# Performance work log

Measured on AMD Instinct MI355X. Metric: run time of the kernel, lower is better.

Reference implementation:

```python
import jax, jax.numpy as jnp
import numpy as np

NEG = 0.01  # torch leaky_relu default slope


def conv1d(x, w, pad):
    # x: [B, C, L], w: [O, I, K], stride 1, no bias (as in FC-STGNN extractor)
    return jax.lax.conv_general_dilated(x, w, (1,), [(pad, pad)], dimension_numbers=('NCH', 'OIH', 'NCH'))


def maxpool2(x):
    # MaxPool1d(kernel=2, stride=2, padding=1); torch pads with -inf for max
    return jax.lax.reduce_window(x, -jnp.inf, jax.lax.max, (1, 1, 2), (1, 1, 2), ((0, 0), (0, 0), (1, 1)))


def pos_encoding(n, d):
    # standard sinusoidal PE table, rows 0..n-1 (n <= max_len=5000)
    pos = jnp.arange(n, dtype=jnp.float32)[:, None]
    div = jnp.exp(jnp.arange(0, d, 2, dtype=jnp.float32) * (-float(np.log(10000.0)) / d))
    pe = jnp.zeros((n, d), jnp.float32)
    pe = pe.at[:, 0::2].set(jnp.sin(pos * div))
    pe = pe.at[:, 1::2].set(jnp.cos(pos * div))
    return pe


def mpnn_block(x, gw, gb, bng, bnb, tw, tb):
    # GraphConvpoolMPNN_block_v6 with time_length=1, time_window_size=1, stride=1:
    # one window, decay mask = ones, mean-pool over the size-1 time window is identity.
    bs, two_h, N = x.shape
    X = x.reshape(bs, N, two_h)                                   # (bs*num_windows, num_node*tw, input_dim)
    h = X @ gw + gb                                               # Dot_Graph_Construction mapping
    adj = jnp.einsum('bnd,bmd->bnm', h, h)                        # dot-product adjacency
    eye = jnp.eye(N, dtype=X.dtype)
    adj = jax.nn.leaky_relu(adj - eye * 1e8, NEG)
    adj = jax.nn.softmax(adj, axis=-1) + eye
    Xb = X * bng + bnb                                            # BatchNorm1d eval (running mean 0 / var 1)
    out = jax.nn.leaky_relu(jnp.einsum('bnm,bmd->bnd', adj, Xb) @ tw + tb, NEG)  # MPNN_mk k=1
    return out                                                    # [bs, N, hidden]


def setup_inputs() -> dict:
    key = jax.random.key(0)
    ks = jax.random.split(key, 20)
    bs, D, N = 4, 128, 1024
    H, OUT, KS = 64, 32, 8        # lstmhidden_dim, lstmout_dim, conv_kernel
    HID = 64                      # hidden_dim
    TWOH = 2 * HID
    CONV_OUT = 18
    NCLS = 6
    f32 = jnp.float32
    rn = lambda k, s, sc: jax.random.normal(k, s, f32) * sc
    return {
        'x_enc': rn(ks[0], (bs, D, N), 1.0),
        'x_mark_enc': rn(ks[1], (bs, D, 4), 1.0),
        'x_dec': rn(ks[2], (bs, D // 2, N), 1.0),
        'x_mark_dec': rn(ks[3], (bs, D // 2, 4), 1.0),
        'conv_w1': rn(ks[4], (H, 1, KS), 1.0 / np.sqrt(KS)),
        'bn1_g': jnp.ones((H,), f32), 'bn1_b': jnp.zeros((H,), f32),
        'conv_w2': rn(ks[5], (2 * H, H, KS), 1.0 / np.sqrt(H * KS)),
        'bn2_g': jnp.ones((2 * H,), f32), 'bn2_b': jnp.zeros((2 * H,), f32),
        'conv_w3': rn(ks[6], (OUT, 2 * H, KS), 1.0 / np.sqrt(2 * H * KS)),
        'bn3_g': jnp.ones((OUT,), f32), 'bn3_b': jnp.zeros((OUT,), f32),
        'map2_w': rn(ks[7], (OUT * CONV_OUT, TWOH), 1.0 / np.sqrt(OUT * CONV_OUT)),
        'map2_b': jnp.zeros((TWOH,), f32),
        'map2_bn_g': jnp.ones((TWOH,), f32), 'map2_bn_b': jnp.zeros((TWOH,), f32),
        'g1_w': rn(ks[8], (TWOH, TWOH), 1.0 / np.sqrt(TWOH)), 'g1_b': jnp.zeros((TWOH,), f32),
        'm1_bn_g': jnp.ones((TWOH,), f32), 'm1_bn_b': jnp.zeros((TWOH,), f32),
        't1_w': rn(ks[9], (TWOH, HID), 1.0 / np.sqrt(TWOH)), 't1_b': jnp.zeros((HID,), f32),
        'g2_w': rn(ks[10], (TWOH, TWOH), 1.0 / np.sqrt(TWOH)), 'g2_b': jnp.zeros((TWOH,), f32),
        'm2_bn_g': jnp.ones((TWOH,), f32), 'm2_bn_b': jnp.zeros((TWOH,), f32),
        't2_w': rn(ks[11], (TWOH, HID), 1.0 / np.sqrt(TWOH)), 't2_b': jnp.zeros((HID,), f32),
        'fc1_w': rn(ks[12], (HID * 2 * N, TWOH), 1.0 / np.sqrt(HID * 2 * N)), 'fc1_b': jnp.zeros((TWOH,), f32),
        'fc2_w': rn(ks[13], (TWOH, TWOH), 1.0 / np.sqrt(TWOH)), 'fc2_b': jnp.zeros((TWOH,), f32),
        'fc3_w': rn(ks[14], (TWOH, HID), 1.0 / np.sqrt(TWOH)), 'fc3_b': jnp.zeros((HID,), f32),
        'fc4_w': rn(ks[15], (HID, NCLS), 1.0 / np.sqrt(HID)), 'fc4_b': jnp.zeros((NCLS,), f32),
    }


def reference(x_enc, x_mark_enc, x_dec, x_mark_dec,
              conv_w1, bn1_g, bn1_b, conv_w2, bn2_g, bn2_b, conv_w3, bn3_g, bn3_b,
              map2_w, map2_b, map2_bn_g, map2_bn_b,
              g1_w, g1_b, m1_bn_g, m1_bn_b, t1_w, t1_b,
              g2_w, g2_b, m2_bn_g, m2_bn_b, t2_w, t2_b,
              fc1_w, fc1_b, fc2_w, fc2_b, fc3_w, fc3_b, fc4_w, fc4_b):
    bs, D, N = x_enc.shape
    k = conv_w1.shape[-1]
    # nonlin_map: 1D-CNN feature extractor over each (sample, node) signal
    a = jnp.swapaxes(x_enc.reshape(bs * N, D, 1), 1, 2)           # [bs*N, 1, D]
    a = maxpool2(jax.nn.relu(conv1d(a, conv_w1, k // 2) * bn1_g[None, :, None] + bn1_b[None, :, None]))
    a = maxpool2(jax.nn.relu(conv1d(a, conv_w2, 4) * bn2_g[None, :, None] + bn2_b[None, :, None]))
    a = maxpool2(jax.nn.relu(conv1d(a, conv_w3, 4) * bn3_g[None, :, None] + bn3_b[None, :, None]))
    a = a.reshape(bs * N, -1)                                     # [bs*N, lstmout_dim*conv_out]
    # nonlin_map2: Linear + BatchNorm1d (eval mode affine)
    a = (a @ map2_w + map2_b) * map2_bn_g + map2_bn_b             # [bs*N, 2h]
    two_h = a.shape[-1]
    # positional encoding with the exact reshape/transpose traffic of the torch forward
    x = jnp.swapaxes(a.reshape(bs, N, two_h), 1, 2).reshape(bs * N, two_h)
    x = x + pos_encoding(bs * N, two_h)
    x = jnp.swapaxes(x.reshape(bs, N, two_h), 1, 2)               # [bs, 2h, N]
    # two graph MPNN branches
    o1 = mpnn_block(x, g1_w, g1_b, m1_bn_g, m1_bn_b, t1_w, t1_b)
    o2 = mpnn_block(x, g2_w, g2_b, m2_bn_g, m2_bn_b, t2_w, t2_b)
    f = jnp.concatenate([o1.reshape(bs, -1), o2.reshape(bs, -1)], axis=-1)
    # MLP head
    f = jax.nn.relu(f @ fc1_w + fc1_b)
    f = jax.nn.relu(f @ fc2_w + fc2_b)
    f = jax.nn.relu(f @ fc3_w + fc3_b)
    return f @ fc4_w + fc4_b                                      # [bs, n_class]
```

## Files before the change

kernel.cpp:

```cpp
#include <hip/hip_runtime.h>
#include <hip/hip_bf16.h>
#include <math.h>

#define NEG 0.01f
__device__ __forceinline__ float lrelu(float v){ return v > 0.f ? v : NEG*v; }
__device__ __forceinline__ float frelu(float v){ return v > 0.f ? v : 0.f; }

typedef __attribute__((ext_vector_type(8))) short bf16x8;
typedef __attribute__((ext_vector_type(4))) float f32x4;

__device__ __forceinline__ unsigned short f2bf(float x){
    unsigned int u = __float_as_uint(x);
    unsigned int r = (u + 0x7FFFu + ((u>>16)&1u)) >> 16;
    return (unsigned short)r;
}
__device__ __forceinline__ float bf2f(unsigned short h){
    return __uint_as_float(((unsigned int)h) << 16);
}
__device__ __forceinline__ unsigned short F2B(float x){
    __hip_bfloat16 h = __float2bfloat16(x);
    return *reinterpret_cast<unsigned short*>(&h);
}

__global__ __launch_bounds__(256) void k_prep(const float* __restrict__ w2, const float* __restrict__ w3,
    const float* __restrict__ m2w,
    unsigned short* __restrict__ w2s, unsigned short* __restrict__ w3s, unsigned short* __restrict__ m2wbT)
{
    int gid = blockIdx.x*256 + threadIdx.x;
    if (gid < 73728) {
        int j = gid / 576, f = gid % 576;
        m2wbT[gid] = f2bf(m2w[f*128 + j]);
    }
    if (gid < 65536) {
        int jj = gid & 7, q = (gid>>3)&3, o = (gid>>5)&127, ks = (gid>>12)&1, k = gid>>13;
        int c = ks*32 + q*8 + jj;
        w2s[gid] = f2bf(w2[o*512 + c*8 + k]);
    }
    if (gid < 32768) {
        int jj = gid & 7, q = (gid>>3)&3, o = (gid>>5)&31, ks = (gid>>10)&3, k = gid>>12;
        int c = ks*32 + q*8 + jj;
        w3s[gid] = f2bf(w3[o*1024 + c*8 + k]);
    }
}

__global__ __launch_bounds__(256) void k_conv(
    const float* __restrict__ xenc,
    const float* __restrict__ w1, const float* __restrict__ g1, const float* __restrict__ b1,
    const unsigned short* __restrict__ w2s, const float* __restrict__ g2, const float* __restrict__ b2,
    const unsigned short* __restrict__ w3s, const float* __restrict__ g3, const float* __restrict__ b3,
    unsigned short* __restrict__ aflatG)
{
    __shared__ __align__(16) unsigned char smraw[22208];
    float* sigp = (float*)smraw;
    unsigned short* p1T = (unsigned short*)(smraw + 576);
    unsigned short* p2T = (unsigned short*)(smraw + 10304);
    unsigned short* astage = (unsigned short*)(smraw + 21056);

    const int t = threadIdx.x;
    const int s = blockIdx.x;

    {
        unsigned int* zz = (unsigned int*)(smraw + 576);
        for (int i = t; i < 5120; i += 256) zz[i] = 0u;
        if (t < 144) sigp[t] = 0.f;
    }
    __syncthreads();
    if (t < 128) sigp[4 + t] = xenc[(size_t)s*128 + t];
    __syncthreads();

    {
        const int c = t & 63, qg = t >> 6;
        float wr[8];
        #pragma unroll
        for (int k = 0; k < 8; ++k) wr[k] = w1[c*8 + k];
        const float g = g1[c], b = b1[c];
        const int qs = qg*17;
        float win[9];
        {
            int base = 2*qs - 1;
            #pragma unroll
            for (int x = 0; x < 9; ++x) win[x] = (base + x >= 0) ? sigp[base + x] : 0.f;
        }
        #pragma unroll
        for (int j = 0; j < 17; ++j) {
            int q = qs + j;
            float s0 = 0.f, s1 = 0.f;
            #pragma unroll
            for (int k = 0; k < 8; ++k) { s0 += win[k]*wr[k]; s1 += win[k+1]*wr[k]; }
            float v = frelu(s1*g + b);
            if (q > 0) v = fmaxf(v, frelu(s0*g + b));
            if (q < 65) {
                int row = q + 4;
                p1T[row*64 + (((c>>3) ^ (row&7))<<3) + (c&7)] = F2B(v);
            }
            #pragma unroll
            for (int x = 0; x < 7; ++x) win[x] = win[x+2];
            win[7] = sigp[2*q + 8];
            win[8] = sigp[2*q + 9];
        }
    }
    __syncthreads();

    {
        const int wv = t >> 6, l = t & 63, lg = l >> 4, lr = l & 15;
        const int pbase = ((lr & 7) << 1) + (lr >> 3) - 1;
        f32x4 acc[2][5] = {};
        for (int k = 0; k < 8; ++k) {
            for (int ks = 0; ks < 2; ++ks) {
                bf16x8 af[2];
                #pragma unroll
                for (int oi = 0; oi < 2; ++oi) {
                    int o = (wv*2 + oi)*16 + lr;
                    af[oi] = *(const bf16x8*)(w2s + ((((k*2 + ks)*128 + o)*4 + lg)<<3));
                }
                const int q = ks*4 + lg;
                #pragma unroll
                for (int nt = 0; nt < 5; ++nt) {
                    int row = nt*16 + pbase + k; row = row > 75 ? 75 : row;
                    bf16x8 bfv = *(const bf16x8*)(p1T + row*64 + ((q ^ (row&7))<<3));
                    acc[0][nt] = __builtin_amdgcn_mfma_f32_16x16x32_bf16(af[0], bfv, acc[0][nt], 0,0,0);
                    acc[1][nt] = __builtin_amdgcn_mfma_f32_16x16x32_bf16(af[1], bfv, acc[1][nt], 0,0,0);
                }
            }
        }
        float ga[2][4], ba[2][4];
        #pragma unroll
        for (int oi = 0; oi < 2; ++oi)
            #pragma unroll
            for (int r = 0; r < 4; ++r) {
                int o = (wv*2 + oi)*16 + lg*4 + r;
                ga[oi][r] = g2[o]; ba[oi][r] = b2[o];
            }
        #pragma unroll
        for (int oi = 0; oi < 2; ++oi)
            #pragma unroll
            for (int nt = 0; nt < 5; ++nt) {
                int p = nt*16 + pbase;
                bool valid = (p >= 0) && (p <= 65);
                float vv[4];
                #pragma unroll
                for (int r = 0; r < 4; ++r) {
                    float v = frelu(acc[oi][nt][r]*ga[oi][r] + ba[oi][r]);
                    vv[r] = valid ? v : -3.0e38f;
                }
                float pv[4];
                #pragma unroll
                for (int r = 0; r < 4; ++r) pv[r] = fmaxf(vv[r], __shfl_xor(vv[r], 8));
                int q = nt*8 + (lr & 7);
                if ((lr >> 3) == 0 && q < 34) {
                    int row2 = q + 4;
                    int o0 = (wv*2 + oi)*16 + lg*4;
                    uint2 pk;
                    pk.x = (unsigned int)F2B(pv[0]) | ((unsigned int)F2B(pv[1]) << 16);
                    pk.y = (unsigned int)F2B(pv[2]) | ((unsigned int)F2B(pv[3]) << 16);
                    *(uint2*)&p2T[row2*128 + (((o0>>3) ^ (row2&15))<<3) + (o0&7)] = pk;
                }
            }
    }
    __syncthreads();

    {
        const int wv = t >> 6, l = t & 63, lg = l >> 4, lr = l & 15;
        const int ot = wv & 1, ntb = (wv >> 1) * 2;
        const int ncnt = (wv < 2) ? 2 : 1;
        const int pbase = ((lr & 7) << 1) + (lr >> 3) - 1;
        f32x4 acc[2] = {};
        for (int k = 0; k < 8; ++k) {
            for (int ks = 0; ks < 4; ++ks) {
                int o = ot*16 + lr;
                bf16x8 af = *(const bf16x8*)(w3s + ((((k*4 + ks)*32 + o)*4 + lg)<<3));
                const int q = ks*4 + lg;
                #pragma unroll
                for (int ni = 0; ni < 2; ++ni) {
                    if (ni < ncnt) {
                        int row = (ntb + ni)*16 + pbase + k; row = row > 41 ? 41 : row;
                        bf16x8 bfv = *(const bf16x8*)(p2T + row*128 + ((q ^ (row&15))<<3));
                        acc[ni] = __builtin_amdgcn_mfma_f32_16x16x32_bf16(af, bfv, acc[ni], 0,0,0);
                    }
                }
            }
        }
        float g3v[4], b3v[4];
        #pragma unroll
        for (int r = 0; r < 4; ++r) {
            int o = ot*16 + lg*4 + r;
            g3v[r] = g3[o]; b3v[r] = b3[o];
        }
        #pragma unroll
        for (int ni = 0; ni < 2; ++ni) if (ni < ncnt) {
            int p = (ntb + ni)*16 + pbase;
            bool valid = (p >= 0) && (p <= 34);
            float vv[4];
            #pragma unroll
            for (int r = 0; r < 4; ++r) {
                float v = frelu(acc[ni][r]*g3v[r] + b3v[r]);
                vv[r] = valid ? v : -3.0e38f;
            }
            float pv[4];
            #pragma unroll
            for (int r = 0; r < 4; ++r) pv[r] = fmaxf(vv[r], __shfl_xor(vv[r], 8));
            int q = (ntb + ni)*8 + (lr & 7);
            if ((lr >> 3) == 0 && q < 18) {
                #pragma unroll
                for (int r = 0; r < 4; ++r)
                    astage[(ot*16 + lg*4 + r)*18 + q] = F2B(pv[r]);
            }
        }
    }
    __syncthreads();

    for (int idx = t; idx < 576; idx += 256)
        aflatG[(size_t)s*576 + idx] = astage[idx];
}

__global__ __launch_bounds__(256) void k_map2(const unsigned short* __restrict__ aflatG,
    const unsigned short* __restrict__ m2wbT,
    const float* __restrict__ m2b, const float* __restrict__ m2g, const float* __restrict__ m2bb,
    float* __restrict__ a2)
{
    const int t = threadIdx.x, wv = t>>6, l = t&63, lg = l>>4, lr = l&15;
    const int s0 = blockIdx.x*64;
    f32x4 acc[8] = {};
    for (int ks = 0; ks < 18; ++ks) {
        bf16x8 a = *(const bf16x8*)(aflatG + (size_t)(s0 + wv*16 + lr)*576 + ks*32 + lg*8);
        #pragma unroll
        for (int nt = 0; nt < 8; ++nt) {
            bf16x8 b = *(const bf16x8*)(m2wbT + (size_t)(nt*16 + lr)*576 + ks*32 + lg*8);
            acc[nt] = __builtin_amdgcn_mfma_f32_16x16x32_bf16(a, b, acc[nt], 0,0,0);
        }
    }
    #pragma unroll
    for (int nt = 0; nt < 8; ++nt)
        #pragma unroll
        for (int r = 0; r < 4; ++r) {
            int s2 = s0 + wv*16 + lg*4 + r;
            int j = nt*16 + lr;
            a2[(size_t)s2*128 + j] = (acc[nt][r] + m2b[j]) * m2g[j] + m2bb[j];
        }
}

__global__ __launch_bounds__(256) void k_buildx(const float* __restrict__ a2, float* __restrict__ X)
{
    __shared__ double dvt[64];
    const int t = threadIdx.x;
    if (t < 64) dvt[t] = exp((double)(2*t) * (-9.210340371976184/128.0));
    __syncthreads();
    int e = blockIdx.x*256 + t;
    int b = e >> 17;
    int r = e & 131071;
    int i = r >> 7, d = r & 127;
    int row = b*1024 + (d & 7)*128 + (i >> 3);
    int col = (i & 7)*16 + (d >> 3);
    float v = a2[row*128 + col];
    int per = b*1024 + (i & 7)*128 + d;
    int pc  = i >> 3;
    double ang = (double)per * dvt[pc >> 1];
    const double TWO_PI = 6.283185307179586476925287;
    double kk = floor(ang * (1.0/TWO_PI) + 0.5);
    float red = (float)(ang - kk * TWO_PI);
    float pe = (pc & 1) ? __cosf(red) : __sinf(red);
    X[e] = v + pe;
}

__global__ __launch_bounds__(256) void k_hmat(const float* __restrict__ X,
    const float* __restrict__ g1w, const float* __restrict__ g1b,
    const float* __restrict__ g2w, const float* __restrict__ g2b,
    unsigned short* __restrict__ Hbhi1, unsigned short* __restrict__ Hblo1,
    unsigned short* __restrict__ Hbhi2, unsigned short* __restrict__ Hblo2)
{
    const int br = blockIdx.y;
    const float* gw = br ? g2w : g1w;
    const float* gb = br ? g2b : g1b;
    unsigned short* Hh = br ? Hbhi2 : Hbhi1;
    unsigned short* Hl = br ? Hblo2 : Hblo1;
    int e = blockIdx.x*256 + threadIdx.x;
    int srow = e >> 7, j = e & 127;
    const float* xr = X + (size_t)srow*128;
    float acc = gb[j];
    for (int k = 0; k < 128; ++k) acc += xr[k] * gw[k*128 + j];
    unsigned short hh = f2bf(acc);
    Hh[e] = hh;
    Hl[e] = f2bf(acc - bf2f(hh));
}

__global__ __launch_bounds__(256) void k_scores(
    const unsigned short* __restrict__ Hbhi, const unsigned short* __restrict__ Hblo,
    float* __restrict__ S)
{
    __shared__ __align__(16) unsigned short HiH[64*64];
    __shared__ __align__(16) unsigned short HiL[64*64];
    __shared__ __align__(16) unsigned short HjH[64*64];
    __shared__ __align__(16) unsigned short HjL[64*64];
    const int b = blockIdx.z;
    const int i0 = blockIdx.y * 64, j0 = blockIdx.x * 64;
    const int t = threadIdx.x;
    const int w = t >> 6, l = t & 63, lr = l & 15, h = l >> 4;
    const size_t hb = (size_t)b * 1024 * 128;

    f32x4 acc[4] = {};
    for (int kh = 0; kh < 2; ++kh) {
        __syncthreads();
        #pragma unroll
        for (int it = 0; it < 4; ++it) {
            int g = it*256 + t;
            int mat = g >> 9;
            int gg = g & 511;
            int row = gg >> 3, ch = gg & 7;
            int base0 = mat ? j0 : i0;
            size_t src = hb + (size_t)(base0 + row)*128 + kh*64 + ch*8;
            uint4 vh = *(const uint4*)(Hbhi + src);
            uint4 vl = *(const uint4*)(Hblo + src);
            int sw = ch ^ (row & 7);
            unsigned short* dh = (mat ? HjH : HiH) + row*64 + sw*8;
            unsigned short* dl = (mat ? HjL : HiL) + row*64 + sw*8;
            *(uint4*)dh = vh;
            *(uint4*)dl = vl;
        }
        __syncthreads();
        #pragma unroll
        for (int kc = 0; kc < 2; ++kc) {
            int swA = (((kc*4 + h) ^ (lr & 7)) << 3);
            bf16x8 ah = *(const bf16x8*)&HiH[(w*16 + lr)*64 + swA];
            bf16x8 al = *(const bf16x8*)&HiL[(w*16 + lr)*64 + swA];
            #pragma unroll
            for (int jt = 0; jt < 4; ++jt) {
                bf16x8 bh = *(const bf16x8*)&HjH[(jt*16 + lr)*64 + swA];
                bf16x8 bl = *(const bf16x8*)&HjL[(jt*16 + lr)*64 + swA];
                acc[jt] = __builtin_amdgcn_mfma_f32_16x16x32_bf16(ah, bh, acc[jt], 0,0,0);
                acc[jt] = __builtin_amdgcn_mfma_f32_16x16x32_bf16(ah, bl, acc[jt], 0,0,0);
                acc[jt] = __builtin_amdgcn_mfma_f32_16x16x32_bf16(al, bh, acc[jt], 0,0,0);
            }
        }
    }
    float* Sb = S + (size_t)b*1024*1024;
    #pragma unroll
    for (int jt = 0; jt < 4; ++jt) {
        #pragma unroll
        for (int r = 0; r < 4; ++r) {
            int i = i0 + w*16 + h*4 + r;
            int j = j0 + jt*16 + lr;
            float x = acc[jt][r];
            if (i == j) x -= 1e8f;
            Sb[(size_t)i*1024 + j] = lrelu(x);
        }
    }
}

__global__ __launch_bounds__(256) void k_rowstat(const float* __restrict__ S,
                                                 float* __restrict__ mrow, float* __restrict__ linv)
{
    __shared__ float red[256];
    const int b = blockIdx.y, i = blockIdx.x, t = threadIdx.x;
    const float* row = S + (size_t)b*1024*1024 + (size_t)i*1024;
    float4 v = *(const float4*)&row[t*4];
    float mx = fmaxf(fmaxf(v.x,v.y), fmaxf(v.z,v.w));
    red[t] = mx; __syncthreads();
    for (int s2 = 128; s2 > 0; s2 >>= 1) { if (t < s2) red[t] = fmaxf(red[t], red[t+s2]); __syncthreads(); }
    mx = red[0]; __syncthreads();
    float e = (__expf(v.x-mx) + __expf(v.y-mx)) + (__expf(v.z-mx) + __expf(v.w-mx));
    red[t] = e; __syncthreads();
    for (int s2 = 128; s2 > 0; s2 >>= 1) { if (t < s2) red[t] += red[t+s2]; __syncthreads(); }
    if (t == 0) { mrow[b*1024 + i] = mx; linv[b*1024 + i] = 1.f / red[0]; }
}

__global__ __launch_bounds__(256) void k_xbbt(const float* __restrict__ X,
    const float* __restrict__ bng1, const float* __restrict__ bnb1,
    const float* __restrict__ bng2, const float* __restrict__ bnb2,
    unsigned short* __restrict__ XbbThi, unsigned short* __restrict__ XbbTlo)
{
    __shared__ float Xl[64][132];
    const int t = threadIdx.x;
    const int j0 = blockIdx.x*64, b = blockIdx.y, br = blockIdx.z;
    {
        int r2 = t >> 2, dseg = (t & 3)*32;
        const float* src = X + ((size_t)(b*1024 + j0 + r2))*128 + dseg;
        #pragma unroll
        for (int q = 0; q < 8; ++q) {
            float4 v = *(const float4*)(src + q*4);
            Xl[r2][dseg + q*4 + 0] = v.x;
            Xl[r2][dseg + q*4 + 1] = v.y;
            Xl[r2][dseg + q*4 + 2] = v.z;
            Xl[r2][dseg + q*4 + 3] = v.w;
        }
    }
    __syncthreads();
    const int d = t >> 1, seg = t & 1;
    const float g  = (br ? bng2 : bng1)[d];
    const float bb = (br ? bnb2 : bnb1)[d];
    unsigned short* dsth = XbbThi + (size_t)br*524288 + ((size_t)(b*128 + d))*1024 + j0 + seg*32;
    unsigned short* dstl = XbbTlo + (size_t)br*524288 + ((size_t)(b*128 + d))*1024 + j0 + seg*32;
    #pragma unroll
    for (int g8 = 0; g8 < 4; ++g8) {
        unsigned int hu[4], lu[4];
        #pragma unroll
        for (int q = 0; q < 4; ++q) {
            float v0 = Xl[seg*32 + g8*8 + 2*q    ][d]*g + bb;
            float v1 = Xl[seg*32 + g8*8 + 2*q + 1][d]*g + bb;
            unsigned short h0 = f2bf(v0), h1 = f2bf(v1);
            hu[q] = (unsigned int)h0 | ((unsigned int)h1 << 16);
            lu[q] = (unsigned int)f2bf(v0 - bf2f(h0)) | ((unsigned int)f2bf(v1 - bf2f(h1)) << 16);
        }
        *(uint4*)(dsth + g8*8) = make_uint4(hu[0],hu[1],hu[2],hu[3]);
        *(uint4*)(dstl + g8*8) = make_uint4(lu[0],lu[1],lu[2],lu[3]);
    }
}

__global__ __launch_bounds__(256) void k_pvmm(
    const float* __restrict__ S1, const float* __restrict__ S2, const float* __restrict__ X,
    const float* __restrict__ bng1, const float* __restrict__ bnb1,
    const float* __restrict__ bng2, const float* __restrict__ bnb2,
    const float* __restrict__ mrow, const float* __restrict__ linv,
    const unsigned short* __restrict__ XbbThi, const unsigned short* __restrict__ XbbTlo,
    float* __restrict__ P)
{
    __shared__ __align__(16) unsigned short ElH[16*64];
    __shared__ __align__(16) unsigned short ElL[16*64];
    const int t = threadIdx.x;
    const int w = t >> 6, l = t & 63, lr = l & 15, h = l >> 4;
    const int i0 = blockIdx.x * 16;
    const int b = blockIdx.y;
    const int br = blockIdx.z;
    const float* S = br ? S2 : S1;
    const float* bng = br ? bng2 : bng1;
    const float* bnb = br ? bnb2 : bnb1;
    const float* mr = mrow + br*4096 + b*1024;
    const float* lv = linv + br*4096 + b*1024;
    const unsigned short* Bh = XbbThi + (size_t)br*524288 + (size_t)b*131072;
    const unsigned short* Bl = XbbTlo + (size_t)br*524288 + (size_t)b*131072;

    const int srow = t >> 4, jseg = t & 15;
    const float mi = mr[i0 + srow];
    const int j0s = jseg*4;
    const int eoff = srow*64 + (((j0s>>3) ^ (srow&7))<<3) + (j0s&7);

    f32x4 acc[2] = {};
    for (int ch = 0; ch < 16; ++ch) {
        const int jb = ch*64;
        __syncthreads();
        {
            float4 sv = *(const float4*)(S + ((size_t)(b*1024 + i0 + srow))*1024 + jb + j0s);
            float e0 = __expf(sv.x - mi), e1 = __expf(sv.y - mi);
            float e2 = __expf(sv.z - mi), e3 = __expf(sv.w - mi);
            unsigned short h0 = f2bf(e0), h1 = f2bf(e1), h2 = f2bf(e2), h3 = f2bf(e3);
            uint2 vh, vl;
            vh.x = (unsigned int)h0 | ((unsigned int)h1 << 16);
            vh.y = (unsigned int)h2 | ((unsigned int)h3 << 16);
            vl.x = (unsigned int)f2bf(e0 - bf2f(h0)) | ((unsigned int)f2bf(e1 - bf2f(h1)) << 16);
            vl.y = (unsigned int)f2bf(e2 - bf2f(h2)) | ((unsigned int)f2bf(e3 - bf2f(h3)) << 16);
            *(uint2*)(ElH + eoff) = vh;
            *(uint2*)(ElL + eoff) = vl;
        }
        __syncthreads();
        #pragma unroll
        for (int kc = 0; kc < 2; ++kc) {
            int swA = (((kc*4 + h) ^ (lr & 7)) << 3);
            bf16x8 ah = *(const bf16x8*)&ElH[lr*64 + swA];
            bf16x8 al = *(const bf16x8*)&ElL[lr*64 + swA];
            #pragma unroll
            for (int n2 = 0; n2 < 2; ++n2) {
                int nt = w*2 + n2;
                size_t boff = (size_t)(nt*16 + lr)*1024 + jb + kc*32 + h*8;
                bf16x8 bh = *(const bf16x8*)(Bh + boff);
                bf16x8 bl = *(const bf16x8*)(Bl + boff);
                acc[n2] = __builtin_amdgcn_mfma_f32_16x16x32_bf16(ah, bh, acc[n2], 0,0,0);
                acc[n2] = __builtin_amdgcn_mfma_f32_16x16x32_bf16(ah, bl, acc[n2], 0,0,0);
                acc[n2] = __builtin_amdgcn_mfma_f32_16x16x32_bf16(al, bh, acc[n2], 0,0,0);
            }
        }
    }
    #pragma unroll
    for (int r = 0; r < 4; ++r) {
        int i = i0 + h*4 + r;
        float inv = lv[i];
        #pragma unroll
        for (int n2 = 0; n2 < 2; ++n2) {
            int d = (w*2 + n2)*16 + lr;
            float xv = X[((size_t)(b*1024 + i))*128 + d] * bng[d] + bnb[d];
            P[((size_t)(br*4096 + b*1024 + i))*128 + d] = acc[n2][r]*inv + xv;
        }
    }
}

__global__ __launch_bounds__(256) void k_pv(const float* __restrict__ S, const float* __restrict__ X,
                                            const float* __restrict__ bng, const float* __restrict__ bnb,
                                            const float* __restrict__ mrowG, const float* __restrict__ linvG,
                                            float* __restrict__ P)
{
    __shared__ __align__(16) float Sl[16*65];
    __shared__ __align__(16) float Xl[64*132];
    const int b = blockIdx.y, i0 = blockIdx.x*16, t = threadIdx.x;
    const int il = t >> 4, dg = t & 15;
    const int sj = t & 63, sil = t >> 6;
    const int xd = t & 127, xj = t >> 7;
    const float bg = bng[xd], bb = bnb[xd];
    float mr[4];
    #pragma unroll
    for (int m2 = 0; m2 < 4; ++m2) mr[m2] = mrowG[b*1024 + i0 + sil*4 + m2];
    float acc[8] = {};
    const float* Sb = S + (size_t)b*1024*1024;
    const float* Xb = X + (size_t)b*1024*128;
    for (int c = 0; c < 16; ++c) {
        int jb = c*64;
        __syncthreads();
        #pragma unroll
        for (int m2 = 0; m2 < 4; ++m2) {
            int r2 = sil*4 + m2;
            Sl[r2*65 + sj] = __expf(Sb[(size_t)(i0+r2)*1024 + jb + sj] - mr[m2]);
        }
        #pragma unroll
        for (int m2 = 0; m2 < 32; ++m2) {
            int jc = xj + 2*m2;
            Xl[jc*132 + xd] = Xb[(size_t)(jb+jc)*128 + xd] * bg + bb;
        }
        __syncthreads();
        for (int jc = 0; jc < 64; ++jc) {
            float sv = Sl[il*65 + jc];
            float4 x0 = *(const float4*)&Xl[jc*132 + dg*8];
            float4 x1 = *(const float4*)&Xl[jc*132 + dg*8 + 4];
            acc[0] += sv*x0.x; acc[1] += sv*x0.y; acc[2] += sv*x0.z; acc[3] += sv*x0.w;
            acc[4] += sv*x1.x; acc[5] += sv*x1.y; acc[6] += sv*x1.z; acc[7] += sv*x1.w;
        }
    }
    int i = i0 + il;
    float inv = linvG[b*1024 + i];
    const float* xr = Xb + (size_t)i*128 + dg*8;
    float* pr = P + (size_t)(b*1024 + i)*128 + dg*8;
    #pragma unroll
    for (int z = 0; z < 8; ++z) {
        float xv = xr[z] * bng[dg*8+z] + bnb[dg*8+z];
        pr[z] = acc[z]*inv + xv;
    }
}

__global__ __launch_bounds__(256) void k_tproj(const float* __restrict__ P, const float* __restrict__ tw,
                                               const float* __restrict__ tb, float* __restrict__ O)
{
    int idx = blockIdx.x*256 + threadIdx.x;
    int srow = idx >> 6, e = idx & 63;
    const float* pr = P + (size_t)srow*128;
    float acc = tb[e];
    for (int d = 0; d < 128; ++d) acc += pr[d] * tw[d*64 + e];
    O[idx] = lrelu(acc);
}

__global__ __launch_bounds__(256) void k_tproj2(const float* __restrict__ P,
    const float* __restrict__ t1w, const float* __restrict__ t1b,
    const float* __restrict__ t2w, const float* __restrict__ t2b,
    float* __restrict__ O)
{
    int idx = blockIdx.x*256 + threadIdx.x;
    int srow = idx >> 6, e = idx & 63;
    int br = srow >> 12;
    const float* tw = br ? t2w : t1w;
    const float* tb = br ? t2b : t1b;
    const float* pr = P + (size_t)srow*128;
    float acc = tb[e];
    for (int d = 0; d < 128; ++d) acc += pr[d] * tw[d*64 + e];
    O[idx] = lrelu(acc);
}

__global__ __launch_bounds__(256) void k_fc1(const float* __restrict__ O1, const float* __restrict__ O2,
                                             const float* __restrict__ w, float* __restrict__ pbuf)
{
    __shared__ float red[4*512];
    const int t = threadIdx.x;
    const int wv = t >> 6, l = t & 63;
    const int gwid = blockIdx.x*4 + wv;
    float acc[4][2] = {};
    int base = gwid*64;
    for (int tt = 0; tt < 64; ++tt) {
        int row = base + tt;
        float2 wvv = *(const float2*)&w[(size_t)row*128 + l*2];
        #pragma unroll
        for (int b = 0; b < 4; ++b) {
            float fb = (row < 65536) ? O1[b*65536 + row] : O2[b*65536 + row - 65536];
            acc[b][0] += fb * wvv.x;
            acc[b][1] += fb * wvv.y;
        }
    }
    #pragma unroll
    for (int b = 0; b < 4; ++b) {
        red[wv*512 + b*128 + l*2]   = acc[b][0];
        red[wv*512 + b*128 + l*2+1] = acc[b][1];
    }
    __syncthreads();
    for (int rep = 0; rep < 2; ++rep) {
        int col = rep*256 + t;
        pbuf[(size_t)blockIdx.x*512 + col] = red[col] + red[512+col] + red[1024+col] + red[1536+col];
    }
}

__global__ __launch_bounds__(256) void k_red(const float* __restrict__ pbuf, float* __restrict__ pbuf2)
{
    int col = blockIdx.x*8 + (threadIdx.x >> 5);
    int lane = threadIdx.x & 31;
    float acc = 0.f;
    for (int it = 0; it < 16; ++it)
        acc += pbuf[(size_t)(lane + it*32)*512 + col];
    #pragma unroll
    for (int s2 = 16; s2 >= 1; s2 >>= 1) acc += __shfl_xor(acc, s2, 32);
    if (lane == 0) pbuf2[col] = acc;
}

__global__ __launch_bounds__(256) void k_head2(const float* __restrict__ pbuf2,
    const float* __restrict__ fc1b, const float* __restrict__ fc2w, const float* __restrict__ fc2b,
    const float* __restrict__ fc3w, const float* __restrict__ fc3b,
    const float* __restrict__ fc4w, const float* __restrict__ fc4b,
    float* __restrict__ out)
{
    __shared__ float r1[512], r2[512], r3[256];
    const int t = threadIdx.x;
    for (int rep = 0; rep < 2; ++rep) {
        int idx = rep*256 + t;
        r1[idx] = frelu(pbuf2[idx] + fc1b[idx & 127]);
    }
    __syncthreads();
    for (int rep = 0; rep < 2; ++rep) {
        int idx = rep*256 + t;
        int b = idx >> 7, j = idx & 127;
        float acc = fc2b[j];
        for (int k = 0; k < 128; ++k) acc += r1[b*128+k]*fc2w[k*128+j];
        r2[idx] = frelu(acc);
    }
    __syncthreads();
    {
        int b = t >> 6, e2 = t & 63;
        float acc = fc3b[e2];
        for (int k = 0; k < 128; ++k) acc += r2[b*128+k]*fc3w[k*64+e2];
        r3[t] = frelu(acc);
    }
    __syncthreads();
    if (t < 24) {
        int b = t/6, c = t%6;
        float acc = fc4b[c];
        for (int k = 0; k < 64; ++k) acc += r3[b*64+k]*fc4w[k*6+c];
        out[b*6+c] = acc;
    }
}

extern "C" void kernel_launch(void* const* d_in, const int* in_sizes, int n_in,
                              void* d_out, int out_size, void* d_ws, size_t ws_size,
                              hipStream_t stream)
{
    (void)in_sizes; (void)n_in; (void)out_size;
    const float* xenc = (const float*)d_in[0];
    const float* w1   = (const float*)d_in[4];
    const float* g1   = (const float*)d_in[5];
    const float* b1   = (const float*)d_in[6];
    const float* w2   = (const float*)d_in[7];
    const float* g2   = (const float*)d_in[8];
    const float* b2   = (const float*)d_in[9];
    const float* w3   = (const float*)d_in[10];
    const float* g3   = (const float*)d_in[11];
    const float* b3   = (const float*)d_in[12];
    const float* m2w  = (const float*)d_in[13];
    const float* m2b  = (const float*)d_in[14];
    const float* m2g  = (const float*)d_in[15];
    const float* m2bb = (const float*)d_in[16];
    const float* g1w  = (const float*)d_in[17];
    const float* g1b  = (const float*)d_in[18];
    const float* m1g  = (const float*)d_in[19];
    const float* m1b  = (const float*)d_in[20];
    const float* t1w  = (const float*)d_in[21];
    const float* t1b  = (const float*)d_in[22];
    const float* g2w  = (const float*)d_in[23];
    const float* g2bv = (const float*)d_in[24];
    const float* mm2g = (const float*)d_in[25];
    const float* mm2b = (const float*)d_in[26];
    const float* t2w  = (const float*)d_in[27];
    const float* t2b  = (const float*)d_in[28];
    const float* fc1w = (const float*)d_in[29];
    const float* fc1b = (const float*)d_in[30];
    const float* fc2w = (const float*)d_in[31];
    const float* fc2b = (const float*)d_in[32];
    const float* fc3w = (const float*)d_in[33];
    const float* fc3b = (const float*)d_in[34];
    const float* fc4w = (const float*)d_in[35];
    const float* fc4b = (const float*)d_in[36];

    char* ws = (char*)d_ws;
    float* a2   = (float*)(ws);
    float* X    = (float*)(ws + (2u<<20));
    unsigned short* Hbhi1 = (unsigned short*)(ws + (4u<<20));
    unsigned short* Hblo1 = (unsigned short*)(ws + (5u<<20));
    unsigned short* Hbhi2 = (unsigned short*)(ws);
    unsigned short* Hblo2 = (unsigned short*)(ws + (1u<<20));
    float* S1   = (float*)(ws + (6u<<20));
    unsigned short* aflatG = (unsigned short*)(ws + (6u<<20));
    unsigned short* w2s    = (unsigned short*)(ws + (6u<<20) + 5242880);
    unsigned short* w3s    = (unsigned short*)(ws + (6u<<20) + 5242880 + 131072);
    unsigned short* m2wbT  = (unsigned short*)(ws + (6u<<20) + 5242880 + 196608);
    float* pbuf2 = (float*)(ws + (6u<<20));

    k_prep<<<288, 256, 0, stream>>>(w2, w3, m2w, w2s, w3s, m2wbT);
    k_conv<<<4096, 256, 0, stream>>>(xenc, w1,g1,b1, w2s,g2,b2, w3s,g3,b3, aflatG);
    k_map2<<<64, 256, 0, stream>>>(aflatG, m2wbT, m2b, m2g, m2bb, a2);
    k_buildx<<<2048, 256, 0, stream>>>(a2, X);
    k_hmat<<<dim3(2048,2), 256, 0, stream>>>(X, g1w, g1b, g2w, g2bv,
                                             Hbhi1, Hblo1, Hbhi2, Hblo2);

    if (ws_size >= ((size_t)49 << 20)) {
        float* S2   = (float*)(ws + (22u<<20));
        float* P    = (float*)(ws + (38u<<20));
        float* O    = (float*)(ws + (42u<<20));
        float* pbuf = (float*)(ws + (44u<<20));
        float* mrow = (float*)(ws + (44u<<20));
        float* linv = (float*)(ws + (44u<<20) + 65536);
        unsigned short* XbbThi = (unsigned short*)(ws + (45u<<20));
        unsigned short* XbbTlo = (unsigned short*)(ws + (47u<<20));
        float* O1 = O;
        float* O2 = O + 262144;

        k_xbbt<<<dim3(16,4,2), 256, 0, stream>>>(X, m1g, m1b, mm2g, mm2b, XbbThi, XbbTlo);
        k_scores <<<dim3(16,16,4), 256, 0, stream>>>(Hbhi1, Hblo1, S1);
        k_scores <<<dim3(16,16,4), 256, 0, stream>>>(Hbhi2, Hblo2, S2);
        k_rowstat<<<dim3(1024,4), 256, 0, stream>>>(S1, mrow, linv);
        k_rowstat<<<dim3(1024,4), 256, 0, stream>>>(S2, mrow + 4096, linv + 4096);
        k_pvmm<<<dim3(64,4,2), 256, 0, stream>>>(S1, S2, X, m1g, m1b, mm2g, mm2b,
                                                 mrow, linv, XbbThi, XbbTlo, P);
        k_tproj2<<<2048, 256, 0, stream>>>(P, t1w, t1b, t2w, t2b, O);
        k_fc1 <<<512, 256, 0, stream>>>(O1, O2, fc1w, pbuf);
        k_red <<<64, 256, 0, stream>>>(pbuf, pbuf2);
        k_head2<<<1, 256, 0, stream>>>(pbuf2, fc1b, fc2w, fc2b, fc3w, fc3b, fc4w, fc4b, (float*)d_out);
    } else {
        float* P    = (float*)(ws + (22u<<20));
        float* O1   = (float*)(ws + (24u<<20));
        float* O2   = (float*)(ws + (25u<<20));
        float* pbuf = (float*)(ws + (26u<<20));
        float* mrow = (float*)(ws + (26u<<20));
        float* linv = (float*)(ws + (26u<<20) + 65536);

        k_scores <<<dim3(16,16,4), 256, 0, stream>>>(Hbhi1, Hblo1, S1);
        k_rowstat<<<dim3(1024,4), 256, 0, stream>>>(S1, mrow, linv);
        k_pv     <<<dim3(64,4), 256, 0, stream>>>(S1, X, m1g, m1b, mrow, linv, P);
        k_tproj  <<<1024, 256, 0, stream>>>(P, t1w, t1b, O1);
        k_scores <<<dim3(16,16,4), 256, 0, stream>>>(Hbhi2, Hblo2, S1);
        k_rowstat<<<dim3(1024,4), 256, 0, stream>>>(S1, mrow, linv);
        k_pv     <<<dim3(64,4), 256, 0, stream>>>(S1, X, mm2g, mm2b, mrow, linv, P);
        k_tproj  <<<1024, 256, 0, stream>>>(P, t2w, t2b, O2);
        k_fc1 <<<512, 256, 0, stream>>>(O1, O2, fc1w, pbuf);
        k_red <<<64, 256, 0, stream>>>(pbuf, pbuf2);
        k_head2<<<1, 256, 0, stream>>>(pbuf2, fc1b, fc2w, fc2b, fc3w, fc3b, fc4w, fc4b, (float*)d_out);
    }
}
```

Before: 279.0 us.

## Use split-bf16 MFMA for temporal projection and merge branch score/rowstat launches

The scalar fp32 temporal-projection kernel is replaced with an MFMA kernel. The PV kernel now writes its output as hi/lo bf16 pairs, and the projection weights are transposed and split into hi/lo bf16 in the prep kernel, so three MFMAs per k-chunk keep accuracy close to fp32. The two branch launches of the score kernel and of the row-statistics kernel are each merged into one launch via the grid z/y dimension, which cuts launch count and improves occupancy. The cost is extra hi/lo traffic for P and some rounding error from dropping the lo*lo product.

```diff
diff --git a/kernel.cpp b/kernel.cpp
--- a/kernel.cpp
+++ b/kernel.cpp
@@ -23,8 +23,9 @@
 }
 
 __global__ __launch_bounds__(256) void k_prep(const float* __restrict__ w2, const float* __restrict__ w3,
-    const float* __restrict__ m2w,
-    unsigned short* __restrict__ w2s, unsigned short* __restrict__ w3s, unsigned short* __restrict__ m2wbT)
+    const float* __restrict__ m2w, const float* __restrict__ t1w, const float* __restrict__ t2w,
+    unsigned short* __restrict__ w2s, unsigned short* __restrict__ w3s, unsigned short* __restrict__ m2wbT,
+    unsigned short* __restrict__ twThi, unsigned short* __restrict__ twTlo)
 {
     int gid = blockIdx.x*256 + threadIdx.x;
     if (gid < 73728) {
@@ -40,6 +41,13 @@
         int jj = gid & 7, q = (gid>>3)&3, o = (gid>>5)&31, ks = (gid>>10)&3, k = gid>>12;
         int c = ks*32 + q*8 + jj;
         w3s[gid] = f2bf(w3[o*1024 + c*8 + k]);
+    }
+    if (gid < 16384) {
+        int d = gid & 127, e = (gid>>7)&63, br = gid>>13;
+        float x = (br ? t2w : t1w)[d*64 + e];
+        unsigned short hh = f2bf(x);
+        twThi[gid] = hh;
+        twTlo[gid] = f2bf(x - bf2f(hh));
     }
 }
 
@@ -284,14 +292,19 @@
 }
 
 __global__ __launch_bounds__(256) void k_scores(
-    const unsigned short* __restrict__ Hbhi, const unsigned short* __restrict__ Hblo,
-    float* __restrict__ S)
+    const unsigned short* __restrict__ Hbhi1, const unsigned short* __restrict__ Hblo1,
+    const unsigned short* __restrict__ Hbhi2, const unsigned short* __restrict__ Hblo2,
+    float* __restrict__ S1, float* __restrict__ S2)
 {
     __shared__ __align__(16) unsigned short HiH[64*64];
     __shared__ __align__(16) unsigned short HiL[64*64];
     __shared__ __align__(16) unsigned short HjH[64*64];
     __shared__ __align__(16) unsigned short HjL[64*64];
-    const int b = blockIdx.z;
+    const int z = blockIdx.z;
+    const int b = z & 3, br = z >> 2;
+    const unsigned short* Hbhi = br ? Hbhi2 : Hbhi1;
+    const unsigned short* Hblo = br ? Hblo2 : Hblo1;
+    float* S = br ? S2 : S1;
     const int i0 = blockIdx.y * 64, j0 = blockIdx.x * 64;
     const int t = threadIdx.x;
     const int w = t >> 6, l = t & 63, lr = l & 15, h = l >> 4;
@@ -346,12 +359,13 @@
     }
 }
 
-__global__ __launch_bounds__(256) void k_rowstat(const float* __restrict__ S,
+__global__ __launch_bounds__(256) void k_rowstat(const float* __restrict__ S1, const float* __restrict__ S2,
                                                  float* __restrict__ mrow, float* __restrict__ linv)
 {
     __shared__ float red[256];
-    const int b = blockIdx.y, i = blockIdx.x, t = threadIdx.x;
-    const float* row = S + (size_t)b*1024*1024 + (size_t)i*1024;
+    const int y = blockIdx.y, i = blockIdx.x, t = threadIdx.x;
+    const int b = y & 3, br = y >> 2;
+    const float* row = (br ? S2 : S1) + (size_t)b*1024*1024 + (size_t)i*1024;
     float4 v = *(const float4*)&row[t*4];
     float mx = fmaxf(fmaxf(v.x,v.y), fmaxf(v.z,v.w));
     red[t] = mx; __syncthreads();
@@ -360,7 +374,7 @@
     float e = (__expf(v.x-mx) + __expf(v.y-mx)) + (__expf(v.z-mx) + __expf(v.w-mx));
     red[t] = e; __syncthreads();
     for (int s2 = 128; s2 > 0; s2 >>= 1) { if (t < s2) red[t] += red[t+s2]; __syncthreads(); }
-    if (t == 0) { mrow[b*1024 + i] = mx; linv[b*1024 + i] = 1.f / red[0]; }
+    if (t == 0) { mrow[y*1024 + i] = mx; linv[y*1024 + i] = 1.f / red[0]; }
 }
 
 __global__ __launch_bounds__(256) void k_xbbt(const float* __restrict__ X,
@@ -411,7 +425,7 @@
     const float* __restrict__ bng2, const float* __restrict__ bnb2,
     const float* __restrict__ mrow, const float* __restrict__ linv,
     const unsigned short* __restrict__ XbbThi, const unsigned short* __restrict__ XbbTlo,
-    float* __restrict__ P)
+    unsigned short* __restrict__ Phi, unsigned short* __restrict__ Plo)
 {
     __shared__ __align__(16) unsigned short ElH[16*64];
     __shared__ __align__(16) unsigned short ElL[16*64];
@@ -476,8 +490,44 @@
         for (int n2 = 0; n2 < 2; ++n2) {
             int d = (w*2 + n2)*16 + lr;
             float xv = X[((size_t)(b*1024 + i))*128 + d] * bng[d] + bnb[d];
-            P[((size_t)(br*4096 + b*1024 + i))*128 + d] = acc[n2][r]*inv + xv;
-        }
+            float pv = acc[n2][r]*inv + xv;
+            size_t off = ((size_t)(br*4096 + b*1024 + i))*128 + d;
+            unsigned short hh = f2bf(pv);
+            Phi[off] = hh;
+            Plo[off] = f2bf(pv - bf2f(hh));
+        }
+    }
+}
+
+__global__ __launch_bounds__(256) void k_tprojmm(
+    const unsigned short* __restrict__ Phi, const unsigned short* __restrict__ Plo,
+    const unsigned short* __restrict__ twThi, const unsigned short* __restrict__ twTlo,
+    const float* __restrict__ t1b, const float* __restrict__ t2b,
+    float* __restrict__ O)
+{
+    const int t = threadIdx.x, w = t>>6, l = t&63, lr = l&15, h = l>>4;
+    const int r0 = blockIdx.x*16;
+    const int br = r0 >> 12;
+    f32x4 acc = {};
+    #pragma unroll
+    for (int kc = 0; kc < 4; ++kc) {
+        size_t aoff = (size_t)(r0 + lr)*128 + kc*32 + h*8;
+        bf16x8 ah = *(const bf16x8*)(Phi + aoff);
+        bf16x8 al = *(const bf16x8*)(Plo + aoff);
+        size_t boff = (size_t)(br*64 + w*16 + lr)*128 + kc*32 + h*8;
+        bf16x8 bh = *(const bf16x8*)(twThi + boff);
+        bf16x8 bl = *(const bf16x8*)(twTlo + boff);
+        acc = __builtin_amdgcn_mfma_f32_16x16x32_bf16(ah, bh, acc, 0,0,0);
+        acc = __builtin_amdgcn_mfma_f32_16x16x32_bf16(ah, bl, acc, 0,0,0);
+        acc = __builtin_amdgcn_mfma_f32_16x16x32_bf16(al, bh, acc, 0,0,0);
+    }
+    const float* tb = br ? t2b : t1b;
+    float tbe = tb[w*16 + lr];
+    int rowLocal0 = r0 & 4095;
+    #pragma unroll
+    for (int r = 0; r < 4; ++r) {
+        int row = rowLocal0 + h*4 + r;
+        O[(size_t)br*262144 + (size_t)row*64 + w*16 + lr] = lrelu(acc[r] + tbe);
     }
 }
 
@@ -537,22 +587,6 @@
 {
     int idx = blockIdx.x*256 + threadIdx.x;
     int srow = idx >> 6, e = idx & 63;
-    const float* pr = P + (size_t)srow*128;
-    float acc = tb[e];
-    for (int d = 0; d < 128; ++d) acc += pr[d] * tw[d*64 + e];
-    O[idx] = lrelu(acc);
-}
-
-__global__ __launch_bounds__(256) void k_tproj2(const float* __restrict__ P,
-    const float* __restrict__ t1w, const float* __restrict__ t1b,
-    const float* __restrict__ t2w, const float* __restrict__ t2b,
-    float* __restrict__ O)
-{
-    int idx = blockIdx.x*256 + threadIdx.x;
-    int srow = idx >> 6, e = idx & 63;
-    int br = srow >> 12;
-    const float* tw = br ? t2w : t1w;
-    const float* tb = br ? t2b : t1b;
     const float* pr = P + (size_t)srow*128;
     float acc = tb[e];
     for (int d = 0; d < 128; ++d) acc += pr[d] * tw[d*64 + e];
@@ -692,33 +726,33 @@
     unsigned short* m2wbT  = (unsigned short*)(ws + (6u<<20) + 5242880 + 196608);
     float* pbuf2 = (float*)(ws + (6u<<20));
 
-    k_prep<<<288, 256, 0, stream>>>(w2, w3, m2w, w2s, w3s, m2wbT);
-    k_conv<<<4096, 256, 0, stream>>>(xenc, w1,g1,b1, w2s,g2,b2, w3s,g3,b3, aflatG);
-    k_map2<<<64, 256, 0, stream>>>(aflatG, m2wbT, m2b, m2g, m2bb, a2);
-    k_buildx<<<2048, 256, 0, stream>>>(a2, X);
-    k_hmat<<<dim3(2048,2), 256, 0, stream>>>(X, g1w, g1b, g2w, g2bv,
-                                             Hbhi1, Hblo1, Hbhi2, Hblo2);
-
     if (ws_size >= ((size_t)49 << 20)) {
         float* S2   = (float*)(ws + (22u<<20));
-        float* P    = (float*)(ws + (38u<<20));
+        unsigned short* Phi = (unsigned short*)(ws + (38u<<20));
+        unsigned short* Plo = (unsigned short*)(ws + (40u<<20));
         float* O    = (float*)(ws + (42u<<20));
         float* pbuf = (float*)(ws + (44u<<20));
         float* mrow = (float*)(ws + (44u<<20));
         float* linv = (float*)(ws + (44u<<20) + 65536);
+        unsigned short* twThi = (unsigned short*)(ws + (44u<<20) + 131072);
+        unsigned short* twTlo = (unsigned short*)(ws + (44u<<20) + 196608);
         unsigned short* XbbThi = (unsigned short*)(ws + (45u<<20));
         unsigned short* XbbTlo = (unsigned short*)(ws + (47u<<20));
         float* O1 = O;
         float* O2 = O + 262144;
 
+        k_prep<<<288, 256, 0, stream>>>(w2, w3, m2w, t1w, t2w, w2s, w3s, m2wbT, twThi, twTlo);
+        k_conv<<<4096, 256, 0, stream>>>(xenc, w1,g1,b1, w2s,g2,b2, w3s,g3,b3, aflatG);
+        k_map2<<<64, 256, 0, stream>>>(aflatG, m2wbT, m2b, m2g, m2bb, a2);
+        k_buildx<<<2048, 256, 0, stream>>>(a2, X);
+        k_hmat<<<dim3(2048,2), 256, 0, stream>>>(X, g1w, g1b, g2w, g2bv,
+                                                 Hbhi1, Hblo1, Hbhi2, Hblo2);
         k_xbbt<<<dim3(16,4,2), 256, 0, stream>>>(X, m1g, m1b, mm2g, mm2b, XbbThi, XbbTlo);
-        k_scores <<<dim3(16,16,4), 256, 0, stream>>>(Hbhi1, Hblo1, S1);
-        k_scores <<<dim3(16,16,4), 256, 0, stream>>>(Hbhi2, Hblo2, S2);
-        k_rowstat<<<dim3(1024,4), 256, 0, stream>>>(S1, mrow, linv);
-        k_rowstat<<<dim3(1024,4), 256, 0, stream>>>(S2, mrow + 4096, linv + 4096);
+        k_scores <<<dim3(16,16,8), 256, 0, stream>>>(Hbhi1, Hblo1, Hbhi2, Hblo2, S1, S2);
+        k_rowstat<<<dim3(1024,8), 256, 0, stream>>>(S1, S2, mrow, linv);
         k_pvmm<<<dim3(64,4,2), 256, 0, stream>>>(S1, S2, X, m1g, m1b, mm2g, mm2b,
-                                                 mrow, linv, XbbThi, XbbTlo, P);
-        k_tproj2<<<2048, 256, 0, stream>>>(P, t1w, t1b, t2w, t2b, O);
+                                                 mrow, linv, XbbThi, XbbTlo, Phi, Plo);
+        k_tprojmm<<<512, 256, 0, stream>>>(Phi, Plo, twThi, twTlo, t1b, t2b, O);
         k_fc1 <<<512, 256, 0, stream>>>(O1, O2, fc1w, pbuf);
         k_red <<<64, 256, 0, stream>>>(pbuf, pbuf2);
         k_head2<<<1, 256, 0, stream>>>(pbuf2, fc1b, fc2w, fc2b, fc3w, fc3b, fc4w, fc4b, (float*)d_out);
@@ -729,13 +763,21 @@
         float* pbuf = (float*)(ws + (26u<<20));
         float* mrow = (float*)(ws + (26u<<20));
         float* linv = (float*)(ws + (26u<<20) + 65536);
-
-        k_scores <<<dim3(16,16,4), 256, 0, stream>>>(Hbhi1, Hblo1, S1);
-        k_rowstat<<<dim3(1024,4), 256, 0, stream>>>(S1, mrow, linv);
+        unsigned short* twThi = (unsigned short*)(ws + (26u<<20) + 131072);
+        unsigned short* twTlo = (unsigned short*)(ws + (26u<<20) + 196608);
+
+        k_prep<<<288, 256, 0, stream>>>(w2, w3, m2w, t1w, t2w, w2s, w3s, m2wbT, twThi, twTlo);
+        k_conv<<<4096, 256, 0, stream>>>(xenc, w1,g1,b1, w2s,g2,b2, w3s,g3,b3, aflatG);
+        k_map2<<<64, 256, 0, stream>>>(aflatG, m2wbT, m2b, m2g, m2bb, a2);
+        k_buildx<<<2048, 256, 0, stream>>>(a2, X);
+        k_hmat<<<dim3(2048,2), 256, 0, stream>>>(X, g1w, g1b, g2w, g2bv,
+                                                 Hbhi1, Hblo1, Hbhi2, Hblo2);
+        k_scores <<<dim3(16,16,4), 256, 0, stream>>>(Hbhi1, Hblo1, Hbhi1, Hblo1, S1, S1);
+        k_rowstat<<<dim3(1024,4), 256, 0, stream>>>(S1, S1, mrow, linv);
         k_pv     <<<dim3(64,4), 256, 0, stream>>>(S1, X, m1g, m1b, mrow, linv, P);
         k_tproj  <<<1024, 256, 0, stream>>>(P, t1w, t1b, O1);
-        k_scores <<<dim3(16,16,4), 256, 0, stream>>>(Hbhi2, Hblo2, S1);
-        k_rowstat<<<dim3(1024,4), 256, 0, stream>>>(S1, mrow, linv);
+        k_scores <<<dim3(16,16,4), 256, 0, stream>>>(Hbhi2, Hblo2, Hbhi2, Hblo2, S1, S1);
+        k_rowstat<<<dim3(1024,4), 256, 0, stream>>>(S1, S1, mrow, linv);
         k_pv     <<<dim3(64,4), 256, 0, stream>>>(S1, X, mm2g, mm2b, mrow, linv, P);
         k_tproj  <<<1024, 256, 0, stream>>>(P, t2w, t2b, O2);
         k_fc1 <<<512, 256, 0, stream>>>(O1, O2, fc1w, pbuf);
```

Result: faster. 262.6 us (-5.9%).
